# Kernel tuning notes

Measured on AMD Instinct MI355X. Metric: run time of the kernel, lower is better.

The kernel has to match this reference:

```python
import jax, jax.numpy as jnp
import numpy as np

B, T, C, HS = 8, 2048, 1024, 128


def setup_inputs() -> dict:
    key = jax.random.key(0)
    k1, k2, k3, k4 = jax.random.split(key, 4)
    return {
        "x": jax.random.normal(k1, (B, T, C), dtype=jnp.float32),
        "Wq": jax.random.normal(k2, (C, HS), dtype=jnp.float32) * (C ** -0.5),
        "Wk": jax.random.normal(k3, (C, HS), dtype=jnp.float32) * (C ** -0.5),
        "Wv": jax.random.normal(k4, (C, HS), dtype=jnp.float32) * (C ** -0.5),
    }


def _rope_tables(T, hs):
    # Matches get_rotary_embedding: d = hs//2, theta_i = 10000**(-2*(i-1)/d) for i in 0..d-1
    d = hs // 2
    i = jnp.arange(d, dtype=jnp.float32)
    theta = 10000.0 ** (-2.0 * (i - 1.0) / d)
    ang = jnp.arange(T, dtype=jnp.float32)[:, None] * theta[None, :]  # [T, d]
    return jnp.cos(ang), jnp.sin(ang)


def _rotate(t, c, s):
    # t: [B,T,hs]. Equivalent to t_m @ R_m with block-diag 2x2 rotations [[c,-s],[s,c]]:
    # out[2i] = e*c + o*s ; out[2i+1] = -e*s + o*c
    e, o = t[..., 0::2], t[..., 1::2]
    return jnp.stack([e * c + o * s, -e * s + o * c], axis=-1).reshape(t.shape)


def reference(x, Wq, Wk, Wv):
    Bx, Tx, Cx = x.shape
    hs = Wq.shape[1]
    c, s = _rope_tables(Tx, hs)
    q = _rotate(x @ Wq, c, s)  # [B,T,hs]
    k = _rotate(x @ Wk, c, s)
    v = x @ Wv
    scores = jnp.einsum("bqh,bkh->bqk", q, k) * (hs ** -0.5)  # [B,T,T]
    mask = jnp.tril(jnp.ones((Tx, Tx), dtype=bool))
    scores = jnp.where(mask, scores, -jnp.inf)
    A = jax.nn.softmax(scores, axis=-1)
    return jnp.einsum("bqk,bkh->bqh", A, v)
```

## Files before the change

### kernel.cpp

```cpp
#include <hip/hip_runtime.h>

typedef __bf16 bf16x8 __attribute__((ext_vector_type(8)));
typedef float f32x4 __attribute__((ext_vector_type(4)));

typedef const unsigned int __attribute__((address_space(1)))* gptr_t;
typedef unsigned int __attribute__((address_space(3)))* lptr_t;

static __device__ __forceinline__ unsigned short f2bf(float f){
  __bf16 h = (__bf16)f;
  return __builtin_bit_cast(unsigned short, h);
}
static __device__ __forceinline__ float bf2f(unsigned short h){
  unsigned int u = ((unsigned int)h) << 16;
  return __builtin_bit_cast(float, u);
}

__global__ __launch_bounds__(256) void k_prepw(const float* __restrict__ Wq,
                                               const float* __restrict__ Wk,
                                               const float* __restrict__ Wv,
                                               unsigned short* __restrict__ Wtb){
  int idx = blockIdx.x * 256 + threadIdx.x;
  int m = idx >> 10;
  int k = idx & 1023;
  const float* W = (m < 128) ? Wq : ((m < 256) ? Wk : Wv);
  int n = m & 127;
  Wtb[idx] = f2bf(W[k * 128 + n]);
}

#define QKV_BUFS 12288
__global__ __launch_bounds__(512) void k_qkv(const float* __restrict__ x,
                                             const unsigned short* __restrict__ Wtb,
                                             unsigned short* __restrict__ Qr,
                                             unsigned short* __restrict__ Kr,
                                             unsigned short* __restrict__ Vt){
  __shared__ __align__(16) unsigned short lds[2 * QKV_BUFS];

  int bid0 = blockIdx.x;
  int wg = (bid0 & 7) * 96 + (bid0 >> 3);
  int mblk = wg / 3;
  int nblk = wg - mblk * 3;

  int tid = threadIdx.x;
  int lane = tid & 63, wid = tid >> 6;
  int wm = wid >> 1, wn = wid & 1;
  int g = lane >> 4, lr = lane & 15;

  f32x4 acc[4] = {};
  const float* xbase = x + (size_t)(mblk * 64) * 1024;
  const unsigned short* wbase = Wtb + (size_t)(nblk * 128) * 1024;

  int ar = tid >> 3, ac = tid & 7;
  const float* agp = xbase + (size_t)ar * 1024 + ac * 8;
  int awoff = ar * 128 + ((ac ^ (ar & 7)) << 4);
  int bp = tid & 7;
  int br1 = tid >> 3, br2 = br1 + 64;
  const unsigned short* bgp1 = wbase + (size_t)br1 * 1024 + ((bp ^ (br1 & 7)) << 3);
  const unsigned short* bgp2 = wbase + (size_t)br2 * 1024 + ((bp ^ (br2 & 7)) << 3);
  int bdoff1 = wid * 512;
  int bdoff2 = 4096 + wid * 512;

  {
    unsigned short* sB = lds + 4096;
    __builtin_amdgcn_global_load_lds((gptr_t)(const void*)bgp1,
                                     (lptr_t)(void*)(sB + bdoff1), 16, 0, 0);
    __builtin_amdgcn_global_load_lds((gptr_t)(const void*)bgp2,
                                     (lptr_t)(void*)(sB + bdoff2), 16, 0, 0);
    float4 v0 = *reinterpret_cast<const float4*>(agp);
    float4 v1 = *reinterpret_cast<const float4*>(agp + 4);
    union { bf16x8 h; uint4 u4; } pk;
    pk.h[0] = (__bf16)v0.x; pk.h[1] = (__bf16)v0.y;
    pk.h[2] = (__bf16)v0.z; pk.h[3] = (__bf16)v0.w;
    pk.h[4] = (__bf16)v1.x; pk.h[5] = (__bf16)v1.y;
    pk.h[6] = (__bf16)v1.z; pk.h[7] = (__bf16)v1.w;
    *reinterpret_cast<uint4*>((char*)lds + awoff) = pk.u4;
    __syncthreads();
  }

  int cur = 0;
  float4 fa0, fa1;
  for (int t = 0; t < 16; t++){
    if (t < 15){
      int k0n = (t + 1) * 64;
      unsigned short* sB = lds + (cur ^ 1) * QKV_BUFS + 4096;
      __builtin_amdgcn_global_load_lds((gptr_t)(const void*)(bgp1 + k0n),
                                       (lptr_t)(void*)(sB + bdoff1), 16, 0, 0);
      __builtin_amdgcn_global_load_lds((gptr_t)(const void*)(bgp2 + k0n),
                                       (lptr_t)(void*)(sB + bdoff2), 16, 0, 0);
      fa0 = *reinterpret_cast<const float4*>(agp + k0n);
      fa1 = *reinterpret_cast<const float4*>(agp + k0n + 4);
    }

    {
      const char* cA = (const char*)(lds + cur * QKV_BUFS);
      const char* cB = cA + 8192;
      int arow = wm * 16 + lr;
      int asw = (arow & 7) << 4;
#pragma unroll
      for (int ks = 0; ks < 2; ks++){
        bf16x8 af = *reinterpret_cast<const bf16x8*>(
            cA + arow * 128 + ((ks * 64 + g * 16) ^ asw));
#pragma unroll
        for (int n = 0; n < 4; n++){
          int brow = wn * 64 + n * 16 + lr;
          bf16x8 bn = *reinterpret_cast<const bf16x8*>(
              cB + brow * 128 + ((ks * 64 + g * 16) ^ ((brow & 7) << 4)));
          acc[n] = __builtin_amdgcn_mfma_f32_16x16x32_bf16(af, bn, acc[n], 0, 0, 0);
        }
      }
    }

    if (t < 15){
      union { bf16x8 h; uint4 u4; } pk;
      pk.h[0] = (__bf16)fa0.x; pk.h[1] = (__bf16)fa0.y;
      pk.h[2] = (__bf16)fa0.z; pk.h[3] = (__bf16)fa0.w;
      pk.h[4] = (__bf16)fa1.x; pk.h[5] = (__bf16)fa1.y;
      pk.h[6] = (__bf16)fa1.z; pk.h[7] = (__bf16)fa1.w;
      *reinterpret_cast<uint4*>((char*)(lds + (cur ^ 1) * QKV_BUFS) + awoff) = pk.u4;
    }
    __syncthreads();
    cur ^= 1;
  }

  int row0 = mblk * 64;
  if (nblk < 2){
    unsigned short* sE = lds;
    float scale = nblk ? 1.0f : 0.12751744950370064f;
#pragma unroll
    for (int n = 0; n < 4; n++){
      int col = wn * 64 + n * 16 + lr;
      int i = col >> 1;
      float theta = exp2f(13.287712379549449f * (2.0f - 2.0f * (float)i) * 0.015625f);
      float sgn = (lr & 1) ? -1.0f : 1.0f;
#pragma unroll
      for (int r = 0; r < 4; r++){
        int tl = wm * 16 + g * 4 + r;
        int t = (row0 + tl) & 2047;
        float s, c;
        sincosf((float)t * theta, &s, &c);
        float v = acc[n][r];
        float partner = __shfl_xor(v, 1);
        float res = (v * c + partner * sgn * s) * scale;
        sE[tl * 136 + col] = f2bf(res);
      }
    }
    __syncthreads();
    unsigned short* dst = (nblk ? Kr : Qr) + (size_t)row0 * 128;
#pragma unroll
    for (int p = 0; p < 2; p++){
      int u = tid + p * 512;
      int tl = u >> 4, h0 = (u & 15) * 8;
      uint4 vv = *reinterpret_cast<const uint4*>(&sE[tl * 136 + h0]);
      *reinterpret_cast<uint4*>(dst + (size_t)tl * 128 + h0) = vv;
    }
  } else {
    unsigned short* sE = lds;
#pragma unroll
    for (int n = 0; n < 4; n++){
      int col = wn * 64 + n * 16 + lr;
#pragma unroll
      for (int r = 0; r < 4; r++){
        int tl = wm * 16 + g * 4 + r;
        sE[col * 72 + tl] = f2bf(acc[n][r]);
      }
    }
    __syncthreads();
    int b = row0 >> 11;
    int t0 = row0 & 2047;
#pragma unroll
    for (int p = 0; p < 2; p++){
      int u = tid + p * 512;
      int h = u >> 3, tc = (u & 7) * 8;
      uint4 vv = *reinterpret_cast<const uint4*>(&sE[h * 72 + tc]);
      *reinterpret_cast<uint4*>(Vt + ((size_t)(b * 128 + h)) * 2048 + t0 + tc) = vv;
    }
  }
}

__global__ __launch_bounds__(128) void k_attn_part(const unsigned short* __restrict__ Qr,
                                                   const unsigned short* __restrict__ Kr,
                                                   const unsigned short* __restrict__ Vt,
                                                   unsigned short* __restrict__ Opart,
                                                   float* __restrict__ ml){
  __shared__ __align__(16) unsigned short sK[32][136];
  __shared__ __align__(16) unsigned short sV[128][40];
  __shared__ __align__(16) unsigned short sP[2][16][40];

  int bid = blockIdx.x;
  int b = bid / 160;
  int rem = bid - b * 160;
  int qt, c;
  if (rem < 16)      { qt = rem;                    c = 0; }
  else if (rem < 48) { qt = 16 + ((rem - 16) >> 1); c = (rem - 16) & 1; }
  else if (rem < 96) { int r2 = rem - 48; int d = r2 / 3; qt = 32 + d; c = r2 - 3 * d; }
  else               { int r3 = rem - 96; qt = 48 + (r3 >> 2); c = r3 & 3; }

  int q_base = qt * 32;
  int kv_start = c * 512;
  int kv_end = min(kv_start + 512, q_base + 32);
  int niter = (kv_end - kv_start) >> 5;

  int tid = threadIdx.x, w = tid >> 6, lane = tid & 63;
  int g = lane >> 4, lr = lane & 15;

  int qrow = q_base + w * 16 + lr;
  const unsigned short* qptr = Qr + ((size_t)(b * 2048 + qrow)) * 128;
  bf16x8 qf[4];
#pragma unroll
  for (int hc = 0; hc < 4; hc++)
    qf[hc] = *reinterpret_cast<const bf16x8*>(qptr + hc * 32 + g * 8);

  f32x4 oacc[8] = {};
  float mrow = -1e30f, lrow = 0.0f;

  const unsigned short* Kb = Kr + (size_t)b * 2048 * 128;
  const unsigned short* Vb = Vt + (size_t)b * 128 * 2048;

  for (int it = 0; it < niter; it++){
    int kv0 = kv_start + it * 32;
    __syncthreads();
#pragma unroll
    for (int p = 0; p < 4; p++){
      int idx = tid + p * 128;
      int r = idx >> 4, c8 = (idx & 15) * 8;
      *reinterpret_cast<uint4*>(&sK[r][c8]) =
        *reinterpret_cast<const uint4*>(Kb + (size_t)(kv0 + r) * 128 + c8);
    }
#pragma unroll
    for (int p = 0; p < 4; p++){
      int idx = tid + p * 128;
      int h = idx >> 2, c8 = (idx & 3) * 8;
      *reinterpret_cast<uint4*>(&sV[h][c8]) =
        *reinterpret_cast<const uint4*>(Vb + (size_t)h * 2048 + kv0 + c8);
    }
    __syncthreads();

    f32x4 st[2];
    __builtin_amdgcn_s_setprio(1);
#pragma unroll
    for (int ct = 0; ct < 2; ct++){
      f32x4 a = {0.f, 0.f, 0.f, 0.f};
#pragma unroll
      for (int hc = 0; hc < 4; hc++){
        bf16x8 kf = *reinterpret_cast<const bf16x8*>(&sK[ct * 16 + lr][hc * 32 + g * 8]);
        a = __builtin_amdgcn_mfma_f32_16x16x32_bf16(kf, qf[hc], a, 0, 0, 0);
      }
      st[ct] = a;
    }
    __builtin_amdgcn_s_setprio(0);

    float mx = -1e30f;
#pragma unroll
    for (int ct = 0; ct < 2; ct++){
      int kvb = kv0 + ct * 16 + g * 4;
#pragma unroll
      for (int r = 0; r < 4; r++){
        float s = (kvb + r <= qrow) ? st[ct][r] : -1e30f;
        st[ct][r] = s;
        mx = fmaxf(mx, s);
      }
    }
    mx = fmaxf(mx, __shfl_xor(mx, 16));
    mx = fmaxf(mx, __shfl_xor(mx, 32));
    float m = fmaxf(mrow, mx);
    float alpha = exp2f(mrow - m);

    float rs = 0.0f;
#pragma unroll
    for (int ct = 0; ct < 2; ct++){
      float p0 = exp2f(st[ct][0] - m);
      float p1 = exp2f(st[ct][1] - m);
      float p2 = exp2f(st[ct][2] - m);
      float p3 = exp2f(st[ct][3] - m);
      rs += (p0 + p1) + (p2 + p3);
      uint2 pk;
      pk.x = ((unsigned int)f2bf(p1) << 16) | f2bf(p0);
      pk.y = ((unsigned int)f2bf(p3) << 16) | f2bf(p2);
      *reinterpret_cast<uint2*>(&sP[w][lr][ct * 16 + g * 4]) = pk;
    }
    rs += __shfl_xor(rs, 16);
    rs += __shfl_xor(rs, 32);
    lrow = lrow * alpha + rs;
    mrow = m;

    float af0 = __shfl(alpha, g * 4 + 0);
    float af1 = __shfl(alpha, g * 4 + 1);
    float af2 = __shfl(alpha, g * 4 + 2);
    float af3 = __shfl(alpha, g * 4 + 3);
#pragma unroll
    for (int ht = 0; ht < 8; ht++){
      oacc[ht][0] *= af0;
      oacc[ht][1] *= af1;
      oacc[ht][2] *= af2;
      oacc[ht][3] *= af3;
    }

    bf16x8 pa = *reinterpret_cast<const bf16x8*>(&sP[w][lr][g * 8]);
    __builtin_amdgcn_s_setprio(1);
#pragma unroll
    for (int ht = 0; ht < 8; ht++){
      bf16x8 vf = *reinterpret_cast<const bf16x8*>(&sV[ht * 16 + lr][g * 8]);
      oacc[ht] = __builtin_amdgcn_mfma_f32_16x16x32_bf16(pa, vf, oacc[ht], 0, 0, 0);
    }
    __builtin_amdgcn_s_setprio(0);
  }

  size_t slot = (size_t)(b * 64 + qt) * 4 + c;
  unsigned short* op = Opart + slot * 4096;
  float* mlp = ml + slot * 64;
#pragma unroll
  for (int ht = 0; ht < 8; ht++)
#pragma unroll
    for (int r = 0; r < 4; r++){
      int rowl = w * 16 + g * 4 + r;
      op[rowl * 128 + ht * 16 + lr] = f2bf(oacc[ht][r]);
    }
  if (lane < 16){
    mlp[w * 16 + lr]      = mrow;
    mlp[32 + w * 16 + lr] = lrow;
  }
}

__global__ __launch_bounds__(256) void k_comb(const unsigned short* __restrict__ Opart,
                                              const float* __restrict__ ml,
                                              float* __restrict__ out){
  int bid = blockIdx.x;
  int b = bid >> 6, qt = bid & 63;
  int nck = (qt >> 4) + 1;
  int tid = threadIdx.x;
  int row = tid >> 3;
  int col0 = (tid & 7) * 16;
  size_t slot0 = (size_t)(b * 64 + qt) * 4;

  float m_c[4], l_c[4];
  float M = -1e30f;
#pragma unroll
  for (int c = 0; c < 4; c++) if (c < nck){
    m_c[c] = ml[(slot0 + c) * 64 + row];
    l_c[c] = ml[(slot0 + c) * 64 + 32 + row];
    M = fmaxf(M, m_c[c]);
  }
  float L = 0.0f, wgt[4];
#pragma unroll
  for (int c = 0; c < 4; c++) if (c < nck){
    wgt[c] = exp2f(m_c[c] - M);
    L += wgt[c] * l_c[c];
  }
  float acc[16] = {};
#pragma unroll
  for (int c = 0; c < 4; c++) if (c < nck){
    const unsigned short* src = Opart + (slot0 + c) * 4096 + row * 128 + col0;
    uint4 u0 = *reinterpret_cast<const uint4*>(src);
    uint4 u1 = *reinterpret_cast<const uint4*>(src + 8);
    unsigned int uu[8] = {u0.x, u0.y, u0.z, u0.w, u1.x, u1.y, u1.z, u1.w};
#pragma unroll
    for (int j = 0; j < 8; j++){
      acc[2 * j]     += wgt[c] * bf2f((unsigned short)(uu[j] & 0xFFFF));
      acc[2 * j + 1] += wgt[c] * bf2f((unsigned short)(uu[j] >> 16));
    }
  }
  float invL = 1.0f / L;
  float* dst = out + ((size_t)(b * 2048 + qt * 32 + row)) * 128 + col0;
#pragma unroll
  for (int j = 0; j < 4; j++){
    float4 v = {acc[4 * j] * invL, acc[4 * j + 1] * invL,
                acc[4 * j + 2] * invL, acc[4 * j + 3] * invL};
    *reinterpret_cast<float4*>(dst + 4 * j) = v;
  }
}

extern "C" void kernel_launch(void* const* d_in, const int* in_sizes, int n_in,
                              void* d_out, int out_size, void* d_ws, size_t ws_size,
                              hipStream_t stream) {
  const float* x  = (const float*)d_in[0];
  const float* Wq = (const float*)d_in[1];
  const float* Wk = (const float*)d_in[2];
  const float* Wv = (const float*)d_in[3];
  float* out = (float*)d_out;

  char* ws = (char*)d_ws;
  unsigned short* Wtb   = (unsigned short*)ws;
  unsigned short* Qr    = (unsigned short*)(ws + 786432);
  unsigned short* Kr    = (unsigned short*)(ws + 786432 + 4194304);
  unsigned short* Vt    = (unsigned short*)(ws + 786432 + 2*4194304);
  unsigned short* Opart = (unsigned short*)(ws + 786432 + 3*4194304);
  float* ml             = (float*)(ws + 786432 + 3*4194304 + 16777216);

  hipLaunchKernelGGL(k_prepw, dim3(1536), dim3(256), 0, stream, Wq, Wk, Wv, Wtb);
  hipLaunchKernelGGL(k_qkv,   dim3(768),  dim3(512), 0, stream, x, Wtb, Qr, Kr, Vt);
  hipLaunchKernelGGL(k_attn_part, dim3(1280), dim3(128), 0, stream, Qr, Kr, Vt, Opart, ml);
  hipLaunchKernelGGL(k_comb, dim3(512), dim3(256), 0, stream, Opart, ml, out);
}
```

Measured before the change: 75.16 us.

## Triple-buffer QKV projection GEMM with two-stage-ahead prefetch and explicit waitcnts

Converts the QKV projection kernel's double-buffered LDS pipeline into a triple-buffered one. The W tile is prefetched two k-steps ahead via global_load_lds and the x tile one step ahead through registers. The full __syncthreads is replaced by manual s_waitcnt vmcnt/lgkmcnt plus s_barrier so that outstanding loads can stay in flight across iterations. This hides more global-load latency at the cost of 50% more LDS, which may reduce occupancy, and it relies on hand-counted vmcnt values being correct.

```diff
diff --git a/kernel.cpp b/kernel.cpp
--- a/kernel.cpp
+++ b/kernel.cpp
@@ -33,7 +33,7 @@
                                              unsigned short* __restrict__ Qr,
                                              unsigned short* __restrict__ Kr,
                                              unsigned short* __restrict__ Vt){
-  __shared__ __align__(16) unsigned short lds[2 * QKV_BUFS];
+  __shared__ __align__(16) unsigned short lds[3 * QKV_BUFS];
 
   int bid0 = blockIdx.x;
   int wg = (bid0 & 7) * 96 + (bid0 >> 3);
@@ -56,15 +56,11 @@
   int br1 = tid >> 3, br2 = br1 + 64;
   const unsigned short* bgp1 = wbase + (size_t)br1 * 1024 + ((bp ^ (br1 & 7)) << 3);
   const unsigned short* bgp2 = wbase + (size_t)br2 * 1024 + ((bp ^ (br2 & 7)) << 3);
-  int bdoff1 = wid * 512;
-  int bdoff2 = 4096 + wid * 512;
-
+  int bdoff1 = 4096 + wid * 512;
+  int bdoff2 = 8192 + wid * 512;
+
+  float4 faA, faB;
   {
-    unsigned short* sB = lds + 4096;
-    __builtin_amdgcn_global_load_lds((gptr_t)(const void*)bgp1,
-                                     (lptr_t)(void*)(sB + bdoff1), 16, 0, 0);
-    __builtin_amdgcn_global_load_lds((gptr_t)(const void*)bgp2,
-                                     (lptr_t)(void*)(sB + bdoff2), 16, 0, 0);
     float4 v0 = *reinterpret_cast<const float4*>(agp);
     float4 v1 = *reinterpret_cast<const float4*>(agp + 4);
     union { bf16x8 h; uint4 u4; } pk;
@@ -73,25 +69,39 @@
     pk.h[4] = (__bf16)v1.x; pk.h[5] = (__bf16)v1.y;
     pk.h[6] = (__bf16)v1.z; pk.h[7] = (__bf16)v1.w;
     *reinterpret_cast<uint4*>((char*)lds + awoff) = pk.u4;
-    __syncthreads();
-  }
-
-  int cur = 0;
-  float4 fa0, fa1;
+    __builtin_amdgcn_global_load_lds((gptr_t)(const void*)bgp1,
+                                     (lptr_t)(void*)(lds + bdoff1), 16, 0, 0);
+    __builtin_amdgcn_global_load_lds((gptr_t)(const void*)bgp2,
+                                     (lptr_t)(void*)(lds + bdoff2), 16, 0, 0);
+    faA = *reinterpret_cast<const float4*>(agp + 64);
+    faB = *reinterpret_cast<const float4*>(agp + 64 + 4);
+    unsigned short* b1 = lds + QKV_BUFS;
+    __builtin_amdgcn_global_load_lds((gptr_t)(const void*)(bgp1 + 64),
+                                     (lptr_t)(void*)(b1 + bdoff1), 16, 0, 0);
+    __builtin_amdgcn_global_load_lds((gptr_t)(const void*)(bgp2 + 64),
+                                     (lptr_t)(void*)(b1 + bdoff2), 16, 0, 0);
+    asm volatile("s_waitcnt vmcnt(2) lgkmcnt(0)" ::: "memory");
+    __builtin_amdgcn_s_barrier();
+    __builtin_amdgcn_sched_barrier(0);
+  }
+
   for (int t = 0; t < 16; t++){
-    if (t < 15){
-      int k0n = (t + 1) * 64;
-      unsigned short* sB = lds + (cur ^ 1) * QKV_BUFS + 4096;
+    unsigned short* bufC = lds + (t % 3) * QKV_BUFS;
+    unsigned short* bufN = lds + ((t + 1) % 3) * QKV_BUFS;
+    unsigned short* bufF = lds + ((t + 2) % 3) * QKV_BUFS;
+    float4 fnA = faA, fnB = faB;
+    if (t < 14){
+      int k0n = (t + 2) * 64;
+      fnA = *reinterpret_cast<const float4*>(agp + k0n);
+      fnB = *reinterpret_cast<const float4*>(agp + k0n + 4);
       __builtin_amdgcn_global_load_lds((gptr_t)(const void*)(bgp1 + k0n),
-                                       (lptr_t)(void*)(sB + bdoff1), 16, 0, 0);
+                                       (lptr_t)(void*)(bufF + bdoff1), 16, 0, 0);
       __builtin_amdgcn_global_load_lds((gptr_t)(const void*)(bgp2 + k0n),
-                                       (lptr_t)(void*)(sB + bdoff2), 16, 0, 0);
-      fa0 = *reinterpret_cast<const float4*>(agp + k0n);
-      fa1 = *reinterpret_cast<const float4*>(agp + k0n + 4);
+                                       (lptr_t)(void*)(bufF + bdoff2), 16, 0, 0);
     }
 
     {
-      const char* cA = (const char*)(lds + cur * QKV_BUFS);
+      const char* cA = (const char*)bufC;
       const char* cB = cA + 8192;
       int arow = wm * 16 + lr;
       int asw = (arow & 7) << 4;
@@ -111,15 +121,22 @@
 
     if (t < 15){
       union { bf16x8 h; uint4 u4; } pk;
-      pk.h[0] = (__bf16)fa0.x; pk.h[1] = (__bf16)fa0.y;
-      pk.h[2] = (__bf16)fa0.z; pk.h[3] = (__bf16)fa0.w;
-      pk.h[4] = (__bf16)fa1.x; pk.h[5] = (__bf16)fa1.y;
-      pk.h[6] = (__bf16)fa1.z; pk.h[7] = (__bf16)fa1.w;
-      *reinterpret_cast<uint4*>((char*)(lds + (cur ^ 1) * QKV_BUFS) + awoff) = pk.u4;
-    }
-    __syncthreads();
-    cur ^= 1;
-  }
+      pk.h[0] = (__bf16)faA.x; pk.h[1] = (__bf16)faA.y;
+      pk.h[2] = (__bf16)faA.z; pk.h[3] = (__bf16)faA.w;
+      pk.h[4] = (__bf16)faB.x; pk.h[5] = (__bf16)faB.y;
+      pk.h[6] = (__bf16)faB.z; pk.h[7] = (__bf16)faB.w;
+      *reinterpret_cast<uint4*>((char*)bufN + awoff) = pk.u4;
+
+      if (t < 14)
+        asm volatile("s_waitcnt vmcnt(4) lgkmcnt(0)" ::: "memory");
+      else
+        asm volatile("s_waitcnt vmcnt(0) lgkmcnt(0)" ::: "memory");
+      __builtin_amdgcn_s_barrier();
+      __builtin_amdgcn_sched_barrier(0);
+    }
+    faA = fnA; faB = fnB;
+  }
+  __syncthreads();
 
   int row0 = mblk * 64;
   if (nblk < 2){
```

Measured after the change: 81.75 us. 1.09x slower.
